# Kernel tuning notes

Hardware: AMD Instinct MI355X
Metric: run time of the kernel (lower is better)

Reference implementation:

```python
import jax, jax.numpy as jnp
from jax import lax
import numpy as np

D_IN = 512    # inputdim
HID = 128     # hiddendim
D_INNER = 2 * HID   # 256
D_PROJ = 2 * D_INNER  # 512
N_STATE = 16
R_DT = 8      # ceil(128/16)
B, H, W = 8, 32, 32


def _layernorm(y, g, b):
    mu = y.mean(-1, keepdims=True)
    var = ((y - mu) ** 2).mean(-1, keepdims=True)
    return (y - mu) / jnp.sqrt(var + 1e-5) * g + b


def _ssm(x, xw, dtw, dtb, Al, Dv, g, be):
    # x: [B, D, L] -> y: [B, L, D]  (Mamba selective scan, delta_softplus=True)
    Bb, D, L = x.shape
    n = Al.shape[1]
    xd = jnp.einsum('bdl,kd->blk', x, xw)             # [B,L,R+2N]
    dts = xd[..., :R_DT]
    Bs = xd[..., R_DT:R_DT + n]                        # [B,L,N]
    Cs = xd[..., R_DT + n:]                            # [B,L,N]
    delta = jax.nn.softplus(jnp.einsum('blr,dr->bld', dts, dtw) + dtb)  # [B,L,D]
    A = -jnp.exp(Al)                                   # [D,N]
    xt = x.transpose(0, 2, 1)                          # [B,L,D]
    dA = jnp.exp(delta[..., None] * A)                 # [B,L,D,N]
    dBx = delta[..., None] * Bs[:, :, None, :] * xt[..., None]  # [B,L,D,N]

    def step(h, inp):
        da, dbx, c = inp
        h = h * da + dbx
        return h, jnp.einsum('bdn,bn->bd', h, c)

    h0 = jnp.zeros((Bb, D, n), x.dtype)
    _, ys = lax.scan(step, h0, (dA.transpose(1, 0, 2, 3),
                                dBx.transpose(1, 0, 2, 3),
                                Cs.transpose(1, 0, 2)))
    y = ys.transpose(1, 0, 2) + xt * Dv                # [B,L,D]
    return _layernorm(y, g, be)


def _up2(y, h, w):
    Bb, L, C = y.shape
    img = y.transpose(0, 2, 1).reshape(Bb, C, h, w)
    img = jnp.repeat(jnp.repeat(img, 2, axis=2), 2, axis=3)
    return img.reshape(Bb, C, 4 * L).transpose(0, 2, 1)


def _conv1x1(x, w, b):
    return jnp.einsum('bchw,oc->bohw', x, w) + b[None, :, None, None]


def _conv2s2(x, w, b):
    out = lax.conv_general_dilated(x, w, (2, 2), 'VALID',
                                   dimension_numbers=('NCHW', 'OIHW', 'NCHW'))
    return out + b[None, :, None, None]


def _forward(input_f, in_w, in_b, c1_w, c1_b, c2_w, c2_b, c3_w, c3_b, out_w, out_b,
             xw1, dtw1, dtb1, Al1, Dv1, g1, be1,
             xw2, dtw2, dtb2, Al2, Dv2, g2, be2,
             xw3, dtw3, dtb3, Al3, Dv3, g3, be3):
    xz = _conv1x1(input_f, in_w, in_b)
    x, z = jnp.split(xz, 2, axis=1)
    f1 = _conv1x1(x, c1_w, c1_b)                      # [B,256,H,W]
    f2 = _conv2s2(f1, c2_w, c2_b)                     # [B,256,H/2,W/2]
    f3 = _conv2s2(f2, c3_w, c3_b)                     # [B,256,H/4,W/4]

    Bb, C, h3, w3 = f3.shape
    fx3 = f3.reshape(Bb, C, h3 * w3)
    y3 = _ssm(fx3, xw3, dtw3, dtb3, Al3, Dv3, g3, be3) + \
         jnp.flip(_ssm(jnp.flip(fx3, -1), xw3, dtw3, dtb3, Al3, Dv3, g3, be3), 1)
    y2_ = _up2(y3, h3, w3)

    _, _, h2, w2 = f2.shape
    fx2 = f2.reshape(Bb, C, h2 * w2)
    y2 = _ssm(fx2, xw2, dtw2, dtb2, Al2, Dv2, g2, be2) + \
         jnp.flip(_ssm(jnp.flip(fx2, -1), xw2, dtw2, dtb2, Al2, Dv2, g2, be2), 1) + y2_
    y1_ = _up2(y2, h2, w2)

    _, _, h1, w1 = f1.shape
    fx1 = f1.reshape(Bb, C, h1 * w1)
    # NOTE: source uses fssm1 forward and fssm2 on the flipped sequence
    y1 = _ssm(fx1, xw1, dtw1, dtb1, Al1, Dv1, g1, be1) + \
         jnp.flip(_ssm(jnp.flip(fx1, -1), xw2, dtw2, dtb2, Al2, Dv2, g2, be2), 1) + y1_

    out1 = y1.transpose(0, 2, 1).reshape(Bb, C, h1, w1)
    out = out1 * jax.nn.silu(z)
    return _conv1x1(out, out_w, out_b)


def setup_inputs() -> dict:
    key = jax.random.key(0)
    ks = iter(jax.random.split(key, 64))
    def nrm(shape, s=0.05):
        return (jax.random.normal(next(ks), shape, dtype=jnp.float32) * s)
    inp = {
        'input_f': jax.random.normal(next(ks), (B, D_IN, H, W), dtype=jnp.float32),
        'in_w': nrm((D_PROJ, D_IN)), 'in_b': nrm((D_PROJ,)),
        'c1_w': nrm((D_INNER, D_INNER)), 'c1_b': nrm((D_INNER,)),
        'c2_w': nrm((D_INNER, D_INNER, 2, 2)), 'c2_b': nrm((D_INNER,)),
        'c3_w': nrm((D_INNER, D_INNER, 2, 2)), 'c3_b': nrm((D_INNER,)),
        'out_w': nrm((D_IN, D_INNER)), 'out_b': nrm((D_IN,)),
    }
    Al = jnp.log(jnp.tile(jnp.arange(1, N_STATE + 1, dtype=jnp.float32), (D_INNER, 1)))
    for i in (1, 2, 3):
        inp[f'xw{i}'] = nrm((R_DT + 2 * N_STATE, D_INNER))
        inp[f'dtw{i}'] = nrm((D_INNER, R_DT), s=R_DT ** -0.5)
        inp[f'dtb{i}'] = nrm((D_INNER,)) - 4.0   # inv-softplus of small dt
        inp[f'Al{i}'] = Al
        inp[f'Dv{i}'] = jnp.ones((D_INNER,), jnp.float32)
        inp[f'g{i}'] = jnp.ones((D_INNER,), jnp.float32)
        inp[f'be{i}'] = jnp.zeros((D_INNER,), jnp.float32)
    return inp


def reference(input_f, in_w, in_b, c1_w, c1_b, c2_w, c2_b, c3_w, c3_b, out_w, out_b,
              xw1, dtw1, dtb1, Al1, Dv1, g1, be1,
              xw2, dtw2, dtb2, Al2, Dv2, g2, be2,
              xw3, dtw3, dtb3, Al3, Dv3, g3, be3):
    return _forward(input_f, in_w, in_b, c1_w, c1_b, c2_w, c2_b, c3_w, c3_b, out_w, out_b,
                    xw1, dtw1, dtb1, Al1, Dv1, g1, be1,
                    xw2, dtw2, dtb2, Al2, Dv2, g2, be2,
                    xw3, dtw3, dtb3, Al3, Dv3, g3, be3)
```

## Files before the change

kernel.cpp:

```cpp
#include <hip/hip_runtime.h>
#include <cstddef>

#define DEV static __device__ __forceinline__

typedef __attribute__((ext_vector_type(8))) short short8;
typedef __attribute__((ext_vector_type(4))) float floatx4;

DEV float siluf(float v) { return v / (1.f + expf(-v)); }

DEV unsigned short f2bf(float f) {
  unsigned int u = __float_as_uint(f);
  u += 0x7fff + ((u >> 16) & 1);
  return (unsigned short)(u >> 16);
}

template <int AMT>
DEV float ror_add(float v) {
  int s = __builtin_amdgcn_update_dpp(0, __float_as_int(v), 0x120 | AMT, 0xF, 0xF, false);
  return v + __int_as_float(s);
}

__global__ __launch_bounds__(256) void cvt_w_k(
    const float* __restrict__ in_w, const float* __restrict__ c1_w,
    const float* __restrict__ c2_w, const float* __restrict__ c3_w,
    const float* __restrict__ out_w, const float* __restrict__ xw1,
    const float* __restrict__ xw2, const float* __restrict__ xw3,
    unsigned short* __restrict__ wsW)
{
  int gid = blockIdx.x * 256 + threadIdx.x;
  float v;
  if      (gid < 262144)  v = in_w[gid];
  else if (gid < 327680)  v = c1_w[gid - 262144];
  else if (gid < 589824)  {
    int off = gid - 327680;
    int o = off >> 10, kk = off & 1023, ij = kk >> 8, c = kk & 255;
    v = c2_w[o * 1024 + c * 4 + ij];
  }
  else if (gid < 851968)  {
    int off = gid - 589824;
    int o = off >> 10, kk = off & 1023, ij = kk >> 8, c = kk & 255;
    v = c3_w[o * 1024 + c * 4 + ij];
  }
  else if (gid < 983040)  v = out_w[gid - 851968];
  else if (gid < 993280)  v = xw1[gid - 983040];
  else if (gid < 1003520) v = xw2[gid - 993280];
  else                    v = xw3[gid - 1003520];
  wsW[gid] = f2bf(v);
}

__global__ __launch_bounds__(256) void tcvt_k(const float* __restrict__ in,
                                              unsigned short* __restrict__ outp,
                                              int C, int L)
{
  __shared__ float tile[32][33];
  int b = blockIdx.y;
  int nLt = L >> 5;
  int pt = blockIdx.x % nLt, ct = blockIdx.x / nLt;
  int p0 = pt * 32, c0 = ct * 32;
  int r = threadIdx.x >> 5, cc = threadIdx.x & 31;
#pragma unroll
  for (int i = 0; i < 4; i++) {
    int row = r + 8 * i;
    tile[row][cc] = in[((size_t)b * C + c0 + row) * L + p0 + cc];
  }
  __syncthreads();
#pragma unroll
  for (int i = 0; i < 4; i++) {
    int row = r + 8 * i;
    outp[((size_t)b * L + p0 + row) * C + c0 + cc] = f2bf(tile[cc][row]);
  }
}

__global__ __launch_bounds__(256) void im2col2_k(const unsigned short* __restrict__ f1t,
                                                 unsigned short* __restrict__ outp)
{
  int idx = blockIdx.x * 256 + threadIdx.x;
  int cs = idx & 31, ij = (idx >> 5) & 3, n = (idx >> 7) & 255, b = idx >> 15;
  int i = ij >> 1, j = ij & 1;
  int y = n >> 4, x = n & 15;
  int pix = (2 * y + i) * 32 + 2 * x + j;
  uint4 v = *(const uint4*)&f1t[((size_t)b * 1024 + pix) * 256 + cs * 8];
  *(uint4*)&outp[((size_t)b * 256 + n) * 1024 + ij * 256 + cs * 8] = v;
}

__global__ __launch_bounds__(256) void im2col3_k(const unsigned short* __restrict__ f2t,
                                                 unsigned short* __restrict__ outp)
{
  int idx = blockIdx.x * 256 + threadIdx.x;
  int cs = idx & 31, ij = (idx >> 5) & 3, n = (idx >> 7) & 63, b = idx >> 13;
  int i = ij >> 1, j = ij & 1;
  int y = n >> 3, x = n & 7;
  int pix = (2 * y + i) * 16 + 2 * x + j;
  uint4 v = *(const uint4*)&f2t[((size_t)b * 256 + pix) * 256 + cs * 8];
  *(uint4*)&outp[((size_t)b * 64 + n) * 1024 + ij * 256 + cs * 8] = v;
}

template <int EPI>
__global__ __launch_bounds__(256) void mgemm_k(
    const unsigned short* __restrict__ A, long long sA,
    const unsigned short* __restrict__ B, long long sB,
    const float* __restrict__ bias, float* __restrict__ Y0,
    unsigned short* __restrict__ Yt, float* __restrict__ Ys,
    int M, int N, int K, int Mt, int Nt)
{
  __shared__ __align__(16) unsigned short Ab[128 * 40];
  __shared__ __align__(16) unsigned short Bb[128 * 40];
  int bid = blockIdx.x;
  int tiles = Mt * Nt;
  int bb = bid / tiles;
  int rr = bid - bb * tiles;
  int m0 = (rr / Nt) * 128;
  int n0 = (rr % Nt) * 128;
  const unsigned short* Ap = A + (size_t)bb * sA;
  const unsigned short* Bp = B + (size_t)bb * sB;

  int t = threadIdx.x;
  int lane = t & 63;
  int wm = ((t >> 7) & 1) * 64;
  int wn = ((t >> 6) & 1) * 64;
  int l15 = lane & 15, quad = lane >> 4;

  int srow = t >> 1;
  int shalf = (t & 1) * 16;
  int arow = m0 + srow; if (arow > M - 1) arow = M - 1;
  int brow = n0 + srow; if (brow > N - 1) brow = N - 1;
  const unsigned short* ap = Ap + (size_t)arow * K + shalf;
  const unsigned short* bp = Bp + (size_t)brow * K + shalf;
  unsigned short* as = &Ab[srow * 40 + shalf];
  unsigned short* bs = &Bb[srow * 40 + shalf];

  floatx4 acc[4][4] = {};

  for (int k0 = 0; k0 < K; k0 += 32) {
    uint4 a0 = *(const uint4*)(ap + k0);
    uint4 a1 = *(const uint4*)(ap + k0 + 8);
    uint4 b0 = *(const uint4*)(bp + k0);
    uint4 b1 = *(const uint4*)(bp + k0 + 8);
    __syncthreads();
    *(uint4*)as = a0; *(uint4*)(as + 8) = a1;
    *(uint4*)bs = b0; *(uint4*)(bs + 8) = b1;
    __syncthreads();
    short8 af[4], bf[4];
#pragma unroll
    for (int i = 0; i < 4; i++)
      af[i] = *(const short8*)&Ab[(wm + i * 16 + l15) * 40 + quad * 8];
#pragma unroll
    for (int j = 0; j < 4; j++)
      bf[j] = *(const short8*)&Bb[(wn + j * 16 + l15) * 40 + quad * 8];
#pragma unroll
    for (int i = 0; i < 4; i++)
#pragma unroll
      for (int j = 0; j < 4; j++)
        acc[i][j] = __builtin_amdgcn_mfma_f32_16x16x32_bf16(af[i], bf[j],
                                                            acc[i][j], 0, 0, 0);
  }

  if (EPI == 1) {
    float bn[4]; int nn[4];
#pragma unroll
    for (int j = 0; j < 4; j++) { nn[j] = n0 + wn + j * 16 + l15; bn[j] = bias[nn[j]]; }
#pragma unroll
    for (int i = 0; i < 4; i++) {
      int pixb = m0 + wm + i * 16 + quad * 4;
#pragma unroll
      for (int j = 0; j < 4; j++) {
        int n = nn[j];
        if (n < 256) {
#pragma unroll
          for (int r = 0; r < 4; r++)
            Yt[((size_t)bb * 1024 + pixb + r) * 256 + n] = f2bf(acc[i][j][r] + bn[j]);
        } else {
#pragma unroll
          for (int r = 0; r < 4; r++)
            Ys[((size_t)bb * 1024 + pixb + r) * 256 + (n - 256)] =
                siluf(acc[i][j][r] + bn[j]);
        }
      }
    }
  } else {
#pragma unroll
    for (int i = 0; i < 4; i++) {
      int m = m0 + wm + i * 16 + quad * 4;
#pragma unroll
      for (int j = 0; j < 4; j++) {
        int n = n0 + wn + j * 16 + l15;
        if (m < M && n < N) {
          float vr[4];
#pragma unroll
          for (int r = 0; r < 4; r++)
            vr[r] = acc[i][j][r] + (bias ? bias[m + r] : 0.f);
          float* yp = &Y0[((size_t)bb * M + m) * N + n];
#pragma unroll
          for (int r = 0; r < 4; r++) yp[(size_t)r * N] = vr[r];
          if (EPI == 2) {
            ushort4 o;
            o.x = f2bf(vr[0]); o.y = f2bf(vr[1]); o.z = f2bf(vr[2]); o.w = f2bf(vr[3]);
            *(ushort4*)&Yt[((size_t)bb * N + n) * M + m] = o;
          }
        }
      }
    }
  }
}

__global__ __launch_bounds__(256) void post_all_k(
    const float* __restrict__ xd12, const float* __restrict__ xd2,
    const float* __restrict__ xd3,
    const float* __restrict__ dtw1, const float* __restrict__ dtb1,
    const float* __restrict__ dtw2, const float* __restrict__ dtb2,
    const float* __restrict__ dtw3, const float* __restrict__ dtb3,
    float* __restrict__ d1f, float* __restrict__ bc1f,
    float* __restrict__ d1b, float* __restrict__ bc1b,
    float* __restrict__ d2g, float* __restrict__ bc2,
    float* __restrict__ d3g, float* __restrict__ bc3)
{
  int bid = blockIdx.x;
  const float* xd; int bstride, L; const float *dtw, *dtb; float *dg, *bg;
  int lt, b;
  if (bid < 512) {
    int r = bid; lt = r & 63; b = r >> 6;
    xd = xd12; bstride = 80 * 1024; L = 1024; dtw = dtw1; dtb = dtb1; dg = d1f; bg = bc1f;
  } else if (bid < 1024) {
    int r = bid - 512; lt = r & 63; b = r >> 6;
    xd = xd12 + 40 * 1024; bstride = 80 * 1024; L = 1024; dtw = dtw2; dtb = dtb2; dg = d1b; bg = bc1b;
  } else if (bid < 1152) {
    int r = bid - 1024; lt = r & 15; b = r >> 4;
    xd = xd2; bstride = 40 * 256; L = 256; dtw = dtw2; dtb = dtb2; dg = d2g; bg = bc2;
  } else {
    int r = bid - 1152; lt = r & 3; b = r >> 2;
    xd = xd3; bstride = 40 * 64; L = 64; dtw = dtw3; dtb = dtb3; dg = d3g; bg = bc3;
  }
  int l0 = lt * 16;
  __shared__ float dl[8][16];
  int t = threadIdx.x;
  const float* xb = xd + (size_t)b * bstride + l0;
  if (t < 128) {
    int r = t >> 4, l = t & 15;
    dl[r][l] = xb[(size_t)r * L + l];
  } else {
    int tt = t - 128;
    int c = tt >> 2, seg = tt & 3;
    float4 v = *(const float4*)&xb[(size_t)(8 + c) * L + seg * 4];
    *(float4*)&bg[((size_t)b * 32 + c) * L + l0 + seg * 4] = v;
  }
  __syncthreads();
  int d = t;
  float dtwv[8];
#pragma unroll
  for (int r = 0; r < 8; r++) dtwv[r] = dtw[d * 8 + r];
  float dtbv = dtb[d];
  float spv[16];
#pragma unroll
  for (int l = 0; l < 16; l++) {
    float s = dtbv;
#pragma unroll
    for (int r = 0; r < 8; r++) s += dl[r][l] * dtwv[r];
    spv[l] = fmaxf(s, 0.f) + log1pf(expf(-fabsf(s)));
  }
  float* dout = dg + ((size_t)b * 256 + d) * L + l0;
#pragma unroll
  for (int i = 0; i < 4; i++)
    *(float4*)&dout[4 * i] = make_float4(spv[4 * i], spv[4 * i + 1],
                                         spv[4 * i + 2], spv[4 * i + 3]);
}

#define SCAN_STEPA(DVV, DXV, BVV) {                \
    float e_ = __expf((DVV) * A);                  \
    h = h * e_ + (BVV) * (DXV);                    \
    P *= e_; }

__global__ __launch_bounds__(256) void scanA_k(
    const float* __restrict__ f1, const float* __restrict__ f2,
    const float* __restrict__ d1f, const float* __restrict__ bc1f,
    const float* __restrict__ d1b, const float* __restrict__ bc1b,
    const float* __restrict__ d2,  const float* __restrict__ bc2,
    const float* __restrict__ Al1, const float* __restrict__ Al2,
    float* __restrict__ cP, float* __restrict__ cQ)
{
  __shared__ __align__(16) float lds[48][68];
  int bid = blockIdx.x;
  int sid, tseg, L; const float *xin, *dlp, *bcp, *Alp;
  if (bid < 4096) {
    sid = bid >> 4; tseg = bid & 15; L = 1024; xin = f1;
    if (((sid >> 4) & 1) == 0) { dlp = d1f; bcp = bc1f; Alp = Al1; }
    else                       { dlp = d1b; bcp = bc1b; Alp = Al2; }
  } else {
    int idx = bid - 4096; sid = idx >> 2; tseg = idx & 3; L = 256;
    xin = f2; dlp = d2; bcp = bc2; Alp = Al2;
  }
  int b = sid >> 5, dir = (sid >> 4) & 1, g = sid & 15;
  int t = threadIdx.x, n = t & 15, dloc = t >> 4, d = g * 16 + dloc;
  int mbase = dir ? (L - 64 * (tseg + 1)) : 64 * tseg;

  int r0 = t >> 4, cs = t & 15;
  {
    const float* p0 = dlp + ((size_t)b * 256 + g * 16 + r0) * L + mbase;
    const float* p1 = xin + ((size_t)b * 256 + g * 16 + r0) * L + mbase;
    const float* p2 = bcp + ((size_t)b * 32 + r0) * L + mbase;
    float4 v0 = *(const float4*)(p0 + cs * 4);
    float4 v1 = *(const float4*)(p1 + cs * 4);
    float4 v2 = *(const float4*)(p2 + cs * 4);
    float4 dx = make_float4(v0.x * v1.x, v0.y * v1.y, v0.z * v1.z, v0.w * v1.w);
    *(float4*)&lds[r0][cs * 4]      = v0;
    *(float4*)&lds[16 + r0][cs * 4] = dx;
    *(float4*)&lds[32 + r0][cs * 4] = v2;
  }
  __syncthreads();

  float A = -expf(Alp[d * 16 + n]);
  float h = 0.f, P = 1.f;
  if (dir == 0) {
#pragma unroll
    for (int g4 = 0; g4 < 16; g4++) {
      int cb = 4 * g4;
      float4 dv4 = *(const float4*)&lds[dloc][cb];
      float4 dx4 = *(const float4*)&lds[16 + dloc][cb];
      float4 bv4 = *(const float4*)&lds[32 + n][cb];
      SCAN_STEPA(dv4.x, dx4.x, bv4.x);
      SCAN_STEPA(dv4.y, dx4.y, bv4.y);
      SCAN_STEPA(dv4.z, dx4.z, bv4.z);
      SCAN_STEPA(dv4.w, dx4.w, bv4.w);
    }
  } else {
#pragma unroll
    for (int g4 = 0; g4 < 16; g4++) {
      int cb = 60 - 4 * g4;
      float4 dv4 = *(const float4*)&lds[dloc][cb];
      float4 dx4 = *(const float4*)&lds[16 + dloc][cb];
      float4 bv4 = *(const float4*)&lds[32 + n][cb];
      SCAN_STEPA(dv4.w, dx4.w, bv4.w);
      SCAN_STEPA(dv4.z, dx4.z, bv4.z);
      SCAN_STEPA(dv4.y, dx4.y, bv4.y);
      SCAN_STEPA(dv4.x, dx4.x, bv4.x);
    }
  }
  cP[(size_t)bid * 256 + t] = P;
  cQ[(size_t)bid * 256 + t] = h;
}

__global__ __launch_bounds__(256) void scanB_k(float* __restrict__ cP,
                                               const float* __restrict__ cQ)
{
  int bidx = blockIdx.x, t = threadIdx.x;
  int S, base;
  if (bidx < 256) { S = 16; base = bidx * 16; }
  else            { S = 4;  base = 4096 + (bidx - 256) * 4; }
  float h = 0.f;
  for (int s = 0; s < S; s++) {
    size_t off = (size_t)(base + s) * 256 + t;
    float p = cP[off], q = cQ[off];
    cP[off] = h;
    h = p * h + q;
  }
}

#define SCAN_STEPY(DVV, DXV, BVV, CVV, COL) {      \
    float e_ = __expf((DVV) * A);                  \
    h = h * e_ + (BVV) * (DXV);                    \
    float pp_ = h * (CVV);                         \
    pp_ = ror_add<1>(pp_);                         \
    pp_ = ror_add<2>(pp_);                         \
    pp_ = ror_add<4>(pp_);                         \
    pp_ = ror_add<8>(pp_);                         \
    ysel = (((COL) & 15) == n) ? pp_ : ysel; }

__global__ __launch_bounds__(256) void scanC_k(
    const float* __restrict__ f1, const float* __restrict__ f2, const float* __restrict__ f3,
    const float* __restrict__ d1f, const float* __restrict__ bc1f,
    const float* __restrict__ d1b, const float* __restrict__ bc1b,
    const float* __restrict__ d2,  const float* __restrict__ bc2,
    const float* __restrict__ d3,  const float* __restrict__ bc3,
    float* __restrict__ y1f, float* __restrict__ y1b,
    float* __restrict__ y2f, float* __restrict__ y2b,
    float* __restrict__ y3f, float* __restrict__ y3b,
    const float* __restrict__ Al1, const float* __restrict__ Dv1,
    const float* __restrict__ Al2, const float* __restrict__ Dv2,
    const float* __restrict__ Al3, const float* __restrict__ Dv3,
    const float* __restrict__ cP)
{
  __shared__ __align__(16) float lds[80][68];
  int bid = blockIdx.x;
  int sid, tseg, L, slot; const float *xin, *dlp, *bcp, *Alp, *Dvp; float* yo;
  if (bid < 4096) {
    sid = bid >> 4; tseg = bid & 15; slot = bid; L = 1024; xin = f1;
    if (((sid >> 4) & 1) == 0) { dlp = d1f; bcp = bc1f; Alp = Al1; Dvp = Dv1; yo = y1f; }
    else                       { dlp = d1b; bcp = bc1b; Alp = Al2; Dvp = Dv2; yo = y1b; }
  } else if (bid < 5120) {
    int idx = bid - 4096; sid = idx >> 2; tseg = idx & 3; slot = bid; L = 256;
    xin = f2; dlp = d2; bcp = bc2; Alp = Al2; Dvp = Dv2;
    yo = ((sid >> 4) & 1) ? y2b : y2f;
  } else {
    sid = bid - 5120; tseg = 0; slot = -1; L = 64;
    xin = f3; dlp = d3; bcp = bc3; Alp = Al3; Dvp = Dv3;
    yo = ((sid >> 4) & 1) ? y3b : y3f;
  }
  int b = sid >> 5, dir = (sid >> 4) & 1, g = sid & 15;
  int t = threadIdx.x, n = t & 15, dloc = t >> 4, d = g * 16 + dloc;
  int mbase = dir ? (L - 64 * (tseg + 1)) : 64 * tseg;

  int r0 = t >> 4, cs = t & 15;
  {
    const float* p0 = dlp + ((size_t)b * 256 + g * 16 + r0) * L + mbase;
    const float* p1 = xin + ((size_t)b * 256 + g * 16 + r0) * L + mbase;
    const float* p2 = bcp + ((size_t)b * 32 + r0) * L + mbase;
    const float* p3 = bcp + ((size_t)b * 32 + 16 + r0) * L + mbase;
    float4 v0 = *(const float4*)(p0 + cs * 4);
    float4 v1 = *(const float4*)(p1 + cs * 4);
    float4 v2 = *(const float4*)(p2 + cs * 4);
    float4 v3 = *(const float4*)(p3 + cs * 4);
    float4 dx = make_float4(v0.x * v1.x, v0.y * v1.y, v0.z * v1.z, v0.w * v1.w);
    *(float4*)&lds[r0][cs * 4]      = v0;
    *(float4*)&lds[16 + r0][cs * 4] = dx;
    *(float4*)&lds[32 + r0][cs * 4] = v1;
    *(float4*)&lds[48 + r0][cs * 4] = v2;
    *(float4*)&lds[64 + r0][cs * 4] = v3;
  }
  float A   = -expf(Alp[d * 16 + n]);
  float Dvv = Dvp[d];
  float h = (slot >= 0) ? cP[(size_t)slot * 256 + t] : 0.f;
  __syncthreads();

  float* ybase = yo + ((size_t)b * L + mbase) * 256 + d;
#pragma unroll
  for (int jj0 = 0; jj0 < 64; jj0 += 16) {
    float ysel = 0.f;
    if (dir == 0) {
#pragma unroll
      for (int g4 = 0; g4 < 4; g4++) {
        int cb = jj0 + 4 * g4;
        float4 dv4 = *(const float4*)&lds[dloc][cb];
        float4 dx4 = *(const float4*)&lds[16 + dloc][cb];
        float4 bv4 = *(const float4*)&lds[48 + n][cb];
        float4 cv4 = *(const float4*)&lds[64 + n][cb];
        SCAN_STEPY(dv4.x, dx4.x, bv4.x, cv4.x, cb + 0);
        SCAN_STEPY(dv4.y, dx4.y, bv4.y, cv4.y, cb + 1);
        SCAN_STEPY(dv4.z, dx4.z, bv4.z, cv4.z, cb + 2);
        SCAN_STEPY(dv4.w, dx4.w, bv4.w, cv4.w, cb + 3);
      }
    } else {
#pragma unroll
      for (int g4 = 0; g4 < 4; g4++) {
        int cb = 60 - jj0 - 4 * g4;
        float4 dv4 = *(const float4*)&lds[dloc][cb];
        float4 dx4 = *(const float4*)&lds[16 + dloc][cb];
        float4 bv4 = *(const float4*)&lds[48 + n][cb];
        float4 cv4 = *(const float4*)&lds[64 + n][cb];
        SCAN_STEPY(dv4.w, dx4.w, bv4.w, cv4.w, cb + 3);
        SCAN_STEPY(dv4.z, dx4.z, bv4.z, cv4.z, cb + 2);
        SCAN_STEPY(dv4.y, dx4.y, bv4.y, cv4.y, cb + 1);
        SCAN_STEPY(dv4.x, dx4.x, bv4.x, cv4.x, cb + 0);
      }
    }
    int colbase = dir ? 48 - jj0 : jj0;
    float xsel = lds[32 + dloc][colbase + n];
    ybase[(size_t)(colbase + n) * 256] = ysel + xsel * Dvv;
  }
}

template <int OUTBF>
__global__ __launch_bounds__(256) void ln_combine(
    const float* __restrict__ yf, const float* __restrict__ yb,
    const float* __restrict__ gf, const float* __restrict__ bef,
    const float* __restrict__ gb, const float* __restrict__ beb,
    const float* __restrict__ up, int Wc,
    const float* __restrict__ szT, void* __restrict__ outv,
    int L, int Wf)
{
  int bid = blockIdx.x;
  int b = bid / L;
  int l = bid - b * L;
  int d = threadIdx.x;
  size_t base = ((size_t)b * L + l) * 256 + d;
  float vf = yf[base], vb = yb[base];
  float4 s = make_float4(vf, vf * vf, vb, vb * vb);
#pragma unroll
  for (int m = 1; m < 64; m <<= 1) {
    s.x += __shfl_xor(s.x, m);
    s.y += __shfl_xor(s.y, m);
    s.z += __shfl_xor(s.z, m);
    s.w += __shfl_xor(s.w, m);
  }
  __shared__ float red[4][4];
  int w = threadIdx.x >> 6;
  if ((threadIdx.x & 63) == 0) {
    red[w][0] = s.x; red[w][1] = s.y; red[w][2] = s.z; red[w][3] = s.w;
  }
  __syncthreads();
  float s0 = red[0][0] + red[1][0] + red[2][0] + red[3][0];
  float s1 = red[0][1] + red[1][1] + red[2][1] + red[3][1];
  float s2 = red[0][2] + red[1][2] + red[2][2] + red[3][2];
  float s3 = red[0][3] + red[1][3] + red[2][3] + red[3][3];
  const float inv = 1.f / 256.f;
  float muf = s0 * inv, varf = s1 * inv - muf * muf;
  float mub = s2 * inv, varb = s3 * inv - mub * mub;
  float rf = rsqrtf(varf + 1e-5f);
  float rb = rsqrtf(varb + 1e-5f);
  float v = (vf - muf) * rf * gf[d] + bef[d] + (vb - mub) * rb * gb[d] + beb[d];
  if (up) {
    int y = l / Wf, x = l - y * Wf;
    int lc = (y >> 1) * Wc + (x >> 1);
    v += up[((size_t)b * (L >> 2) + lc) * 256 + d];
  }
  if (szT) v *= szT[base];
  if (OUTBF) ((unsigned short*)outv)[base] = f2bf(v);
  else       ((float*)outv)[base] = v;
}

extern "C" void kernel_launch(void* const* d_in, const int* in_sizes, int n_in,
                              void* d_out, int out_size, void* d_ws, size_t ws_size,
                              hipStream_t stream) {
  (void)in_sizes; (void)n_in; (void)out_size; (void)ws_size;
  const float* input_f = (const float*)d_in[0];
  const float* in_w  = (const float*)d_in[1];
  const float* in_b  = (const float*)d_in[2];
  const float* c1_w  = (const float*)d_in[3];
  const float* c1_b  = (const float*)d_in[4];
  const float* c2_w  = (const float*)d_in[5];
  const float* c2_b  = (const float*)d_in[6];
  const float* c3_w  = (const float*)d_in[7];
  const float* c3_b  = (const float*)d_in[8];
  const float* out_w = (const float*)d_in[9];
  const float* out_b = (const float*)d_in[10];
  const float* xw1  = (const float*)d_in[11];
  const float* dtw1 = (const float*)d_in[12];
  const float* dtb1 = (const float*)d_in[13];
  const float* Al1  = (const float*)d_in[14];
  const float* Dv1  = (const float*)d_in[15];
  const float* g1   = (const float*)d_in[16];
  const float* be1  = (const float*)d_in[17];
  const float* xw2  = (const float*)d_in[18];
  const float* dtw2 = (const float*)d_in[19];
  const float* dtb2 = (const float*)d_in[20];
  const float* Al2  = (const float*)d_in[21];
  const float* Dv2  = (const float*)d_in[22];
  const float* g2   = (const float*)d_in[23];
  const float* be2  = (const float*)d_in[24];
  const float* xw3  = (const float*)d_in[25];
  const float* dtw3 = (const float*)d_in[26];
  const float* dtb3 = (const float*)d_in[27];
  const float* Al3  = (const float*)d_in[28];
  const float* Dv3  = (const float*)d_in[29];
  const float* g3   = (const float*)d_in[30];
  const float* be3  = (const float*)d_in[31];

  float* ws = (float*)d_ws;
  constexpr size_t M1 = 2097152;
  float* d1f = ws;
  unsigned short* xt = (unsigned short*)(ws + M1);
  float* y1f = ws + M1;
  float* szT = ws + 2 * M1;
  float* f1  = ws + 3 * M1;
  unsigned short* G = (unsigned short*)(ws + 3 * M1);
  float* d1b = ws + 4 * M1;
  unsigned short* inT = (unsigned short*)(ws + 5 * M1);
  unsigned short* ic2 = inT;
  unsigned short* f1t = inT + 2097152;
  unsigned short* ic3 = f1t;
  float* y1b = ws + 5 * M1;
  size_t o = 6 * M1;
  float* f2   = ws + o; o += 524288;
  float* f3   = ws + o; o += 131072;
  float* bc1f = ws + o; o += 262144;
  float* bc1b = ws + o; o += 262144;
  float* d2   = ws + o; o += 524288;
  float* bc2  = ws + o; o += 65536;
  float* d3   = ws + o; o += 131072;
  float* bc3  = ws + o; o += 16384;
  float* y2f  = ws + o; o += 524288;
  float* y2b  = ws + o; o += 524288;
  float* y3f  = ws + o; o += 131072;
  float* y3b  = ws + o; o += 131072;
  float* y3c  = ws + o; o += 131072;
  float* y2c  = ws + o; o += 524288;
  float* cP   = ws + o; o += 1310720;
  float* cQ   = ws + o; o += 1310720;
  unsigned short* wsW = (unsigned short*)(ws + o); o += 506880;
  float* xd12 = cP;
  float* xd2  = cP + 655360;
  float* xd3  = cP + 737280;
  unsigned short* f2t = (unsigned short*)cQ;
  unsigned short* f3t = (unsigned short*)(cQ + 262144);
  unsigned short* w_in   = wsW;
  unsigned short* w_c1   = wsW + 262144;
  unsigned short* w_c2   = wsW + 327680;
  unsigned short* w_c3   = wsW + 589824;
  unsigned short* w_out  = wsW + 851968;
  unsigned short* w_xw12 = wsW + 983040;
  unsigned short* w_xw2  = wsW + 993280;
  unsigned short* w_xw3  = wsW + 1003520;

  dim3 blk(256);

  cvt_w_k<<<dim3(3960), blk, 0, stream>>>(in_w, c1_w, c2_w, c3_w, out_w,
                                          xw1, xw2, xw3, wsW);
  tcvt_k<<<dim3(512, 8), blk, 0, stream>>>(input_f, inT, 512, 1024);
  mgemm_k<1><<<dim3(256), blk, 0, stream>>>(inT, 1024 * 512, w_in, 0, in_b,
                                            nullptr, xt, szT, 1024, 512, 512, 8, 4);
  mgemm_k<2><<<dim3(128), blk, 0, stream>>>(w_c1, 0, xt, 1024 * 256, c1_b,
                                            f1, f1t, nullptr, 256, 1024, 256, 2, 8);
  mgemm_k<0><<<dim3(64), blk, 0, stream>>>(w_xw12, 0, f1t, 1024 * 256, nullptr,
                                           xd12, nullptr, nullptr, 80, 1024, 256, 1, 8);
  im2col2_k<<<dim3(1024), blk, 0, stream>>>(f1t, ic2);
  mgemm_k<2><<<dim3(32), blk, 0, stream>>>(w_c2, 0, ic2, 256 * 1024, c2_b,
                                           f2, f2t, nullptr, 256, 256, 1024, 2, 2);
  im2col3_k<<<dim3(256), blk, 0, stream>>>(f2t, ic3);
  mgemm_k<2><<<dim3(16), blk, 0, stream>>>(w_c3, 0, ic3, 64 * 1024, c3_b,
                                           f3, f3t, nullptr, 256, 64, 1024, 2, 1);
  mgemm_k<0><<<dim3(16), blk, 0, stream>>>(w_xw2, 0, f2t, 256 * 256, nullptr,
                                           xd2, nullptr, nullptr, 40, 256, 256, 1, 2);
  mgemm_k<0><<<dim3(8), blk, 0, stream>>>(w_xw3, 0, f3t, 64 * 256, nullptr,
                                          xd3, nullptr, nullptr, 40, 64, 256, 1, 1);
  post_all_k<<<dim3(1184), blk, 0, stream>>>(xd12, xd2, xd3,
                                             dtw1, dtb1, dtw2, dtb2, dtw3, dtb3,
                                             d1f, bc1f, d1b, bc1b, d2, bc2, d3, bc3);
  scanA_k<<<dim3(5120), blk, 0, stream>>>(f1, f2, d1f, bc1f, d1b, bc1b,
                                          d2, bc2, Al1, Al2, cP, cQ);
  scanB_k<<<dim3(512), blk, 0, stream>>>(cP, cQ);
  scanC_k<<<dim3(5376), blk, 0, stream>>>(f1, f2, f3,
                                          d1f, bc1f, d1b, bc1b, d2, bc2, d3, bc3,
                                          y1f, y1b, y2f, y2b, y3f, y3b,
                                          Al1, Dv1, Al2, Dv2, Al3, Dv3, cP);
  ln_combine<0><<<dim3(512), blk, 0, stream>>>(y3f, y3b, g3, be3, g3, be3,
                                               nullptr, 0, nullptr, y3c, 64, 8);
  ln_combine<0><<<dim3(2048), blk, 0, stream>>>(y2f, y2b, g2, be2, g2, be2,
                                                y3c, 8, nullptr, y2c, 256, 16);
  ln_combine<1><<<dim3(8192), blk, 0, stream>>>(y1f, y1b, g1, be1, g2, be2,
                                                y2c, 16, szT, G, 1024, 32);
  mgemm_k<0><<<dim3(256), blk, 0, stream>>>(w_out, 0, G, 1024 * 256, out_b,
                                            (float*)d_out, nullptr, nullptr,
                                            512, 1024, 256, 4, 8);
}
```

Measured before the change: 387.2 us.

## Merge small launches, store activations in bf16, fold carry combine into scan

Merges the weight-conversion and input-transpose kernels into one launch. Runs the im2col copies inside the same launches as the small xd GEMMs. Stores the f1/f2/f3 conv outputs and the SiLU gate as bf16 instead of fp32, which halves their memory traffic. Drops the scanB kernel: each scanC block now combines the preceding segment carries itself and recovers x as dx/delta instead of keeping a separate x tile in LDS. This cuts launch count and bandwidth, but adds redundant serial carry work per block and some extra precision loss from bf16 storage and the division.

```diff
diff --git a/kernel.cpp b/kernel.cpp
--- a/kernel.cpp
+++ b/kernel.cpp
@@ -13,6 +13,12 @@
   u += 0x7fff + ((u >> 16) & 1);
   return (unsigned short)(u >> 16);
 }
+DEV float bf2f(unsigned short u) {
+  return __uint_as_float(((unsigned int)u) << 16);
+}
+DEV float4 bf2f4(ushort4 v) {
+  return make_float4(bf2f(v.x), bf2f(v.y), bf2f(v.z), bf2f(v.w));
+}
 
 template <int AMT>
 DEV float ror_add(float v) {
@@ -20,92 +26,66 @@
   return v + __int_as_float(s);
 }
 
-__global__ __launch_bounds__(256) void cvt_w_k(
+__global__ __launch_bounds__(256) void prep_k(
     const float* __restrict__ in_w, const float* __restrict__ c1_w,
     const float* __restrict__ c2_w, const float* __restrict__ c3_w,
     const float* __restrict__ out_w, const float* __restrict__ xw1,
     const float* __restrict__ xw2, const float* __restrict__ xw3,
-    unsigned short* __restrict__ wsW)
-{
-  int gid = blockIdx.x * 256 + threadIdx.x;
-  float v;
-  if      (gid < 262144)  v = in_w[gid];
-  else if (gid < 327680)  v = c1_w[gid - 262144];
-  else if (gid < 589824)  {
-    int off = gid - 327680;
-    int o = off >> 10, kk = off & 1023, ij = kk >> 8, c = kk & 255;
-    v = c2_w[o * 1024 + c * 4 + ij];
-  }
-  else if (gid < 851968)  {
-    int off = gid - 589824;
-    int o = off >> 10, kk = off & 1023, ij = kk >> 8, c = kk & 255;
-    v = c3_w[o * 1024 + c * 4 + ij];
-  }
-  else if (gid < 983040)  v = out_w[gid - 851968];
-  else if (gid < 993280)  v = xw1[gid - 983040];
-  else if (gid < 1003520) v = xw2[gid - 993280];
-  else                    v = xw3[gid - 1003520];
-  wsW[gid] = f2bf(v);
-}
-
-__global__ __launch_bounds__(256) void tcvt_k(const float* __restrict__ in,
-                                              unsigned short* __restrict__ outp,
-                                              int C, int L)
+    unsigned short* __restrict__ wsW,
+    const float* __restrict__ input_f, unsigned short* __restrict__ inT)
 {
   __shared__ float tile[32][33];
-  int b = blockIdx.y;
-  int nLt = L >> 5;
-  int pt = blockIdx.x % nLt, ct = blockIdx.x / nLt;
-  int p0 = pt * 32, c0 = ct * 32;
-  int r = threadIdx.x >> 5, cc = threadIdx.x & 31;
-#pragma unroll
-  for (int i = 0; i < 4; i++) {
-    int row = r + 8 * i;
-    tile[row][cc] = in[((size_t)b * C + c0 + row) * L + p0 + cc];
-  }
-  __syncthreads();
-#pragma unroll
-  for (int i = 0; i < 4; i++) {
-    int row = r + 8 * i;
-    outp[((size_t)b * L + p0 + row) * C + c0 + cc] = f2bf(tile[cc][row]);
-  }
-}
-
-__global__ __launch_bounds__(256) void im2col2_k(const unsigned short* __restrict__ f1t,
-                                                 unsigned short* __restrict__ outp)
-{
-  int idx = blockIdx.x * 256 + threadIdx.x;
-  int cs = idx & 31, ij = (idx >> 5) & 3, n = (idx >> 7) & 255, b = idx >> 15;
-  int i = ij >> 1, j = ij & 1;
-  int y = n >> 4, x = n & 15;
-  int pix = (2 * y + i) * 32 + 2 * x + j;
-  uint4 v = *(const uint4*)&f1t[((size_t)b * 1024 + pix) * 256 + cs * 8];
-  *(uint4*)&outp[((size_t)b * 256 + n) * 1024 + ij * 256 + cs * 8] = v;
-}
-
-__global__ __launch_bounds__(256) void im2col3_k(const unsigned short* __restrict__ f2t,
-                                                 unsigned short* __restrict__ outp)
-{
-  int idx = blockIdx.x * 256 + threadIdx.x;
-  int cs = idx & 31, ij = (idx >> 5) & 3, n = (idx >> 7) & 63, b = idx >> 13;
-  int i = ij >> 1, j = ij & 1;
-  int y = n >> 3, x = n & 7;
-  int pix = (2 * y + i) * 16 + 2 * x + j;
-  uint4 v = *(const uint4*)&f2t[((size_t)b * 256 + pix) * 256 + cs * 8];
-  *(uint4*)&outp[((size_t)b * 64 + n) * 1024 + ij * 256 + cs * 8] = v;
+  int bid = blockIdx.x;
+  int t = threadIdx.x;
+  if (bid < 3960) {
+    int gid = bid * 256 + t;
+    float v;
+    if      (gid < 262144)  v = in_w[gid];
+    else if (gid < 327680)  v = c1_w[gid - 262144];
+    else if (gid < 589824)  {
+      int off = gid - 327680;
+      int o = off >> 10, kk = off & 1023, ij = kk >> 8, c = kk & 255;
+      v = c2_w[o * 1024 + c * 4 + ij];
+    }
+    else if (gid < 851968)  {
+      int off = gid - 589824;
+      int o = off >> 10, kk = off & 1023, ij = kk >> 8, c = kk & 255;
+      v = c3_w[o * 1024 + c * 4 + ij];
+    }
+    else if (gid < 983040)  v = out_w[gid - 851968];
+    else if (gid < 993280)  v = xw1[gid - 983040];
+    else if (gid < 1003520) v = xw2[gid - 993280];
+    else                    v = xw3[gid - 1003520];
+    wsW[gid] = f2bf(v);
+  } else {
+    int idx = bid - 3960;
+    int b = idx >> 9, blk = idx & 511;
+    int pt = blk & 31, ct = blk >> 5;
+    int p0 = pt * 32, c0 = ct * 32;
+    int r = t >> 5, cc = t & 31;
+#pragma unroll
+    for (int i = 0; i < 4; i++) {
+      int row = r + 8 * i;
+      tile[row][cc] = input_f[((size_t)b * 512 + c0 + row) * 1024 + p0 + cc];
+    }
+    __syncthreads();
+#pragma unroll
+    for (int i = 0; i < 4; i++) {
+      int row = r + 8 * i;
+      inT[((size_t)b * 1024 + p0 + row) * 512 + c0 + cc] = f2bf(tile[cc][row]);
+    }
+  }
 }
 
 template <int EPI>
-__global__ __launch_bounds__(256) void mgemm_k(
-    const unsigned short* __restrict__ A, long long sA,
-    const unsigned short* __restrict__ B, long long sB,
-    const float* __restrict__ bias, float* __restrict__ Y0,
-    unsigned short* __restrict__ Yt, float* __restrict__ Ys,
-    int M, int N, int K, int Mt, int Nt)
+DEV void mgemm_body(const unsigned short* __restrict__ A, long long sA,
+                    const unsigned short* __restrict__ B, long long sB,
+                    const float* __restrict__ bias,
+                    void* __restrict__ O1, void* __restrict__ O2,
+                    int M, int N, int K, int Mt, int Nt, int bid)
 {
   __shared__ __align__(16) unsigned short Ab[128 * 40];
   __shared__ __align__(16) unsigned short Bb[128 * 40];
-  int bid = blockIdx.x;
   int tiles = Mt * Nt;
   int bb = bid / tiles;
   int rr = bid - bb * tiles;
@@ -156,6 +136,8 @@
   }
 
   if (EPI == 1) {
+    unsigned short* Yt = (unsigned short*)O1;
+    unsigned short* Ys = (unsigned short*)O2;
     float bn[4]; int nn[4];
 #pragma unroll
     for (int j = 0; j < 4; j++) { nn[j] = n0 + wn + j * 16 + l15; bn[j] = bias[nn[j]]; }
@@ -173,7 +155,7 @@
 #pragma unroll
           for (int r = 0; r < 4; r++)
             Ys[((size_t)bb * 1024 + pixb + r) * 256 + (n - 256)] =
-                siluf(acc[i][j][r] + bn[j]);
+                f2bf(siluf(acc[i][j][r] + bn[j]));
         }
       }
     }
@@ -189,10 +171,17 @@
 #pragma unroll
           for (int r = 0; r < 4; r++)
             vr[r] = acc[i][j][r] + (bias ? bias[m + r] : 0.f);
-          float* yp = &Y0[((size_t)bb * M + m) * N + n];
-#pragma unroll
-          for (int r = 0; r < 4; r++) yp[(size_t)r * N] = vr[r];
-          if (EPI == 2) {
+          if (EPI == 0) {
+            float* Y0 = (float*)O1;
+            float* yp = &Y0[((size_t)bb * M + m) * N + n];
+#pragma unroll
+            for (int r = 0; r < 4; r++) yp[(size_t)r * N] = vr[r];
+          } else {
+            unsigned short* Y0b = (unsigned short*)O1;
+            unsigned short* Yt  = (unsigned short*)O2;
+#pragma unroll
+            for (int r = 0; r < 4; r++)
+              Y0b[((size_t)bb * M + m + r) * N + n] = f2bf(vr[r]);
             ushort4 o;
             o.x = f2bf(vr[0]); o.y = f2bf(vr[1]); o.z = f2bf(vr[2]); o.w = f2bf(vr[3]);
             *(ushort4*)&Yt[((size_t)bb * N + n) * M + m] = o;
@@ -200,6 +189,54 @@
         }
       }
     }
+  }
+}
+
+template <int EPI>
+__global__ __launch_bounds__(256) void mgemm_k(
+    const unsigned short* __restrict__ A, long long sA,
+    const unsigned short* __restrict__ B, long long sB,
+    const float* __restrict__ bias, void* __restrict__ O1, void* __restrict__ O2,
+    int M, int N, int K, int Mt, int Nt)
+{
+  mgemm_body<EPI>(A, sA, B, sB, bias, O1, O2, M, N, K, Mt, Nt, blockIdx.x);
+}
+
+__global__ __launch_bounds__(256) void fat1_k(
+    const unsigned short* __restrict__ w_xw12, const unsigned short* __restrict__ f1t,
+    float* __restrict__ xd12, unsigned short* __restrict__ ic2)
+{
+  int bid = blockIdx.x;
+  if (bid < 64) {
+    mgemm_body<0>(w_xw12, 0, f1t, 1024 * 256, nullptr, xd12, nullptr,
+                  80, 1024, 256, 1, 8, bid);
+  } else {
+    int idx = (bid - 64) * 256 + threadIdx.x;
+    int cs = idx & 31, ij = (idx >> 5) & 3, n = (idx >> 7) & 255, b = idx >> 15;
+    int i = ij >> 1, j = ij & 1;
+    int y = n >> 4, x = n & 15;
+    int pix = (2 * y + i) * 32 + 2 * x + j;
+    uint4 v = *(const uint4*)&f1t[((size_t)b * 1024 + pix) * 256 + cs * 8];
+    *(uint4*)&ic2[((size_t)b * 256 + n) * 1024 + ij * 256 + cs * 8] = v;
+  }
+}
+
+__global__ __launch_bounds__(256) void fat2_k(
+    const unsigned short* __restrict__ w_xw2, const unsigned short* __restrict__ f2t,
+    float* __restrict__ xd2, unsigned short* __restrict__ ic3)
+{
+  int bid = blockIdx.x;
+  if (bid < 16) {
+    mgemm_body<0>(w_xw2, 0, f2t, 256 * 256, nullptr, xd2, nullptr,
+                  40, 256, 256, 1, 2, bid);
+  } else {
+    int idx = (bid - 16) * 256 + threadIdx.x;
+    int cs = idx & 31, ij = (idx >> 5) & 3, n = (idx >> 7) & 63, b = idx >> 13;
+    int i = ij >> 1, j = ij & 1;
+    int y = n >> 3, x = n & 7;
+    int pix = (2 * y + i) * 16 + 2 * x + j;
+    uint4 v = *(const uint4*)&f2t[((size_t)b * 256 + pix) * 256 + cs * 8];
+    *(uint4*)&ic3[((size_t)b * 64 + n) * 1024 + ij * 256 + cs * 8] = v;
   }
 }
 
@@ -270,7 +307,7 @@
     P *= e_; }
 
 __global__ __launch_bounds__(256) void scanA_k(
-    const float* __restrict__ f1, const float* __restrict__ f2,
+    const unsigned short* __restrict__ f1b, const unsigned short* __restrict__ f2b,
     const float* __restrict__ d1f, const float* __restrict__ bc1f,
     const float* __restrict__ d1b, const float* __restrict__ bc1b,
     const float* __restrict__ d2,  const float* __restrict__ bc2,
@@ -279,14 +316,14 @@
 {
   __shared__ __align__(16) float lds[48][68];
   int bid = blockIdx.x;
-  int sid, tseg, L; const float *xin, *dlp, *bcp, *Alp;
+  int sid, tseg, L; const unsigned short* xin; const float *dlp, *bcp, *Alp;
   if (bid < 4096) {
-    sid = bid >> 4; tseg = bid & 15; L = 1024; xin = f1;
+    sid = bid >> 4; tseg = bid & 15; L = 1024; xin = f1b;
     if (((sid >> 4) & 1) == 0) { dlp = d1f; bcp = bc1f; Alp = Al1; }
     else                       { dlp = d1b; bcp = bc1b; Alp = Al2; }
   } else {
     int idx = bid - 4096; sid = idx >> 2; tseg = idx & 3; L = 256;
-    xin = f2; dlp = d2; bcp = bc2; Alp = Al2;
+    xin = f2b; dlp = d2; bcp = bc2; Alp = Al2;
   }
   int b = sid >> 5, dir = (sid >> 4) & 1, g = sid & 15;
   int t = threadIdx.x, n = t & 15, dloc = t >> 4, d = g * 16 + dloc;
@@ -295,12 +332,12 @@
   int r0 = t >> 4, cs = t & 15;
   {
     const float* p0 = dlp + ((size_t)b * 256 + g * 16 + r0) * L + mbase;
-    const float* p1 = xin + ((size_t)b * 256 + g * 16 + r0) * L + mbase;
+    const unsigned short* p1 = xin + ((size_t)b * 256 + g * 16 + r0) * L + mbase;
     const float* p2 = bcp + ((size_t)b * 32 + r0) * L + mbase;
     float4 v0 = *(const float4*)(p0 + cs * 4);
-    float4 v1 = *(const float4*)(p1 + cs * 4);
+    float4 xf = bf2f4(*(const ushort4*)(p1 + cs * 4));
     float4 v2 = *(const float4*)(p2 + cs * 4);
-    float4 dx = make_float4(v0.x * v1.x, v0.y * v1.y, v0.z * v1.z, v0.w * v1.w);
+    float4 dx = make_float4(v0.x * xf.x, v0.y * xf.y, v0.z * xf.z, v0.w * xf.w);
     *(float4*)&lds[r0][cs * 4]      = v0;
     *(float4*)&lds[16 + r0][cs * 4] = dx;
     *(float4*)&lds[32 + r0][cs * 4] = v2;
@@ -338,22 +375,6 @@
   cQ[(size_t)bid * 256 + t] = h;
 }
 
-__global__ __launch_bounds__(256) void scanB_k(float* __restrict__ cP,
-                                               const float* __restrict__ cQ)
-{
-  int bidx = blockIdx.x, t = threadIdx.x;
-  int S, base;
-  if (bidx < 256) { S = 16; base = bidx * 16; }
-  else            { S = 4;  base = 4096 + (bidx - 256) * 4; }
-  float h = 0.f;
-  for (int s = 0; s < S; s++) {
-    size_t off = (size_t)(base + s) * 256 + t;
-    float p = cP[off], q = cQ[off];
-    cP[off] = h;
-    h = p * h + q;
-  }
-}
-
 #define SCAN_STEPY(DVV, DXV, BVV, CVV, COL) {      \
     float e_ = __expf((DVV) * A);                  \
     h = h * e_ + (BVV) * (DXV);                    \
@@ -365,7 +386,8 @@
     ysel = (((COL) & 15) == n) ? pp_ : ysel; }
 
 __global__ __launch_bounds__(256) void scanC_k(
-    const float* __restrict__ f1, const float* __restrict__ f2, const float* __restrict__ f3,
+    const unsigned short* __restrict__ f1b, const unsigned short* __restrict__ f2b,
+    const unsigned short* __restrict__ f3b,
     const float* __restrict__ d1f, const float* __restrict__ bc1f,
     const float* __restrict__ d1b, const float* __restrict__ bc1b,
     const float* __restrict__ d2,  const float* __restrict__ bc2,
@@ -376,22 +398,23 @@
     const float* __restrict__ Al1, const float* __restrict__ Dv1,
     const float* __restrict__ Al2, const float* __restrict__ Dv2,
     const float* __restrict__ Al3, const float* __restrict__ Dv3,
-    const float* __restrict__ cP)
-{
-  __shared__ __align__(16) float lds[80][68];
+    const float* __restrict__ cP, const float* __restrict__ cQ)
+{
+  __shared__ __align__(16) float lds[64][68];
   int bid = blockIdx.x;
-  int sid, tseg, L, slot; const float *xin, *dlp, *bcp, *Alp, *Dvp; float* yo;
+  int sid, tseg, L, sbase; const unsigned short* xin;
+  const float *dlp, *bcp, *Alp, *Dvp; float* yo;
   if (bid < 4096) {
-    sid = bid >> 4; tseg = bid & 15; slot = bid; L = 1024; xin = f1;
+    sid = bid >> 4; tseg = bid & 15; sbase = sid * 16; L = 1024; xin = f1b;
     if (((sid >> 4) & 1) == 0) { dlp = d1f; bcp = bc1f; Alp = Al1; Dvp = Dv1; yo = y1f; }
     else                       { dlp = d1b; bcp = bc1b; Alp = Al2; Dvp = Dv2; yo = y1b; }
   } else if (bid < 5120) {
-    int idx = bid - 4096; sid = idx >> 2; tseg = idx & 3; slot = bid; L = 256;
-    xin = f2; dlp = d2; bcp = bc2; Alp = Al2; Dvp = Dv2;
+    int idx = bid - 4096; sid = idx >> 2; tseg = idx & 3; sbase = 4096 + sid * 4;
+    L = 256; xin = f2b; dlp = d2; bcp = bc2; Alp = Al2; Dvp = Dv2;
     yo = ((sid >> 4) & 1) ? y2b : y2f;
   } else {
-    sid = bid - 5120; tseg = 0; slot = -1; L = 64;
-    xin = f3; dlp = d3; bcp = bc3; Alp = Al3; Dvp = Dv3;
+    sid = bid - 5120; tseg = 0; sbase = -1; L = 64;
+    xin = f3b; dlp = d3; bcp = bc3; Alp = Al3; Dvp = Dv3;
     yo = ((sid >> 4) & 1) ? y3b : y3f;
   }
   int b = sid >> 5, dir = (sid >> 4) & 1, g = sid & 15;
@@ -401,23 +424,28 @@
   int r0 = t >> 4, cs = t & 15;
   {
     const float* p0 = dlp + ((size_t)b * 256 + g * 16 + r0) * L + mbase;
-    const float* p1 = xin + ((size_t)b * 256 + g * 16 + r0) * L + mbase;
+    const unsigned short* p1 = xin + ((size_t)b * 256 + g * 16 + r0) * L + mbase;
     const float* p2 = bcp + ((size_t)b * 32 + r0) * L + mbase;
     const float* p3 = bcp + ((size_t)b * 32 + 16 + r0) * L + mbase;
     float4 v0 = *(const float4*)(p0 + cs * 4);
-    float4 v1 = *(const float4*)(p1 + cs * 4);
+    float4 xf = bf2f4(*(const ushort4*)(p1 + cs * 4));
     float4 v2 = *(const float4*)(p2 + cs * 4);
     float4 v3 = *(const float4*)(p3 + cs * 4);
-    float4 dx = make_float4(v0.x * v1.x, v0.y * v1.y, v0.z * v1.z, v0.w * v1.w);
+    float4 dx = make_float4(v0.x * xf.x, v0.y * xf.y, v0.z * xf.z, v0.w * xf.w);
     *(float4*)&lds[r0][cs * 4]      = v0;
     *(float4*)&lds[16 + r0][cs * 4] = dx;
-    *(float4*)&lds[32 + r0][cs * 4] = v1;
-    *(float4*)&lds[48 + r0][cs * 4] = v2;
-    *(float4*)&lds[64 + r0][cs * 4] = v3;
+    *(float4*)&lds[32 + r0][cs * 4] = v2;
+    *(float4*)&lds[48 + r0][cs * 4] = v3;
   }
   float A   = -expf(Alp[d * 16 + n]);
   float Dvv = Dvp[d];
-  float h = (slot >= 0) ? cP[(size_t)slot * 256 + t] : 0.f;
+  float h = 0.f;
+  if (sbase >= 0) {
+    for (int s = 0; s < tseg; ++s) {
+      size_t off = (size_t)(sbase + s) * 256 + t;
+      h = cP[off] * h + cQ[off];
+    }
+  }
   __syncthreads();
 
   float* ybase = yo + ((size_t)b * L + mbase) * 256 + d;
@@ -430,8 +458,8 @@
         int cb = jj0 + 4 * g4;
         float4 dv4 = *(const float4*)&lds[dloc][cb];
         float4 dx4 = *(const float4*)&lds[16 + dloc][cb];
-        float4 bv4 = *(const float4*)&lds[48 + n][cb];
-        float4 cv4 = *(const float4*)&lds[64 + n][cb];
+        float4 bv4 = *(const float4*)&lds[32 + n][cb];
+        float4 cv4 = *(const float4*)&lds[48 + n][cb];
         SCAN_STEPY(dv4.x, dx4.x, bv4.x, cv4.x, cb + 0);
         SCAN_STEPY(dv4.y, dx4.y, bv4.y, cv4.y, cb + 1);
         SCAN_STEPY(dv4.z, dx4.z, bv4.z, cv4.z, cb + 2);
@@ -443,8 +471,8 @@
         int cb = 60 - jj0 - 4 * g4;
         float4 dv4 = *(const float4*)&lds[dloc][cb];
         float4 dx4 = *(const float4*)&lds[16 + dloc][cb];
-        float4 bv4 = *(const float4*)&lds[48 + n][cb];
-        float4 cv4 = *(const float4*)&lds[64 + n][cb];
+        float4 bv4 = *(const float4*)&lds[32 + n][cb];
+        float4 cv4 = *(const float4*)&lds[48 + n][cb];
         SCAN_STEPY(dv4.w, dx4.w, bv4.w, cv4.w, cb + 3);
         SCAN_STEPY(dv4.z, dx4.z, bv4.z, cv4.z, cb + 2);
         SCAN_STEPY(dv4.y, dx4.y, bv4.y, cv4.y, cb + 1);
@@ -452,7 +480,9 @@
       }
     }
     int colbase = dir ? 48 - jj0 : jj0;
-    float xsel = lds[32 + dloc][colbase + n];
+    float dsel  = lds[dloc][colbase + n];
+    float dxsel = lds[16 + dloc][colbase + n];
+    float xsel  = dxsel / fmaxf(dsel, 1e-30f);
     ybase[(size_t)(colbase + n) * 256] = ysel + xsel * Dvv;
   }
 }
@@ -463,7 +493,7 @@
     const float* __restrict__ gf, const float* __restrict__ bef,
     const float* __restrict__ gb, const float* __restrict__ beb,
     const float* __restrict__ up, int Wc,
-    const float* __restrict__ szT, void* __restrict__ outv,
+    const unsigned short* __restrict__ szb, void* __restrict__ outv,
     int L, int Wf)
 {
   int bid = blockIdx.x;
@@ -501,7 +531,7 @@
     int lc = (y >> 1) * Wc + (x >> 1);
     v += up[((size_t)b * (L >> 2) + lc) * 256 + d];
   }
-  if (szT) v *= szT[base];
+  if (szb) v *= bf2f(szb[base]);
   if (OUTBF) ((unsigned short*)outv)[base] = f2bf(v);
   else       ((float*)outv)[base] = v;
 }
@@ -548,9 +578,9 @@
   float* d1f = ws;
   unsigned short* xt = (unsigned short*)(ws + M1);
   float* y1f = ws + M1;
-  float* szT = ws + 2 * M1;
-  float* f1  = ws + 3 * M1;
-  unsigned short* G = (unsigned short*)(ws + 3 * M1);
+  unsigned short* szb = (unsigned short*)(ws + 2 * M1);
+  unsigned short* f1b = (unsigned short*)(ws + 3 * M1);
+  unsigned short* G = (unsigned short*)(ws + 3 * M1) + 2097152;
   float* d1b = ws + 4 * M1;
   unsigned short* inT = (unsigned short*)(ws + 5 * M1);
   unsigned short* ic2 = inT;
@@ -558,8 +588,8 @@
   unsigned short* ic3 = f1t;
   float* y1b = ws + 5 * M1;
   size_t o = 6 * M1;
-  float* f2   = ws + o; o += 524288;
-  float* f3   = ws + o; o += 131072;
+  unsigned short* f2b = (unsigned short*)(ws + o); o += 524288;
+  unsigned short* f3b = (unsigned short*)(ws + o); o += 131072;
   float* bc1f = ws + o; o += 262144;
   float* bc1b = ws + o; o += 262144;
   float* d2   = ws + o; o += 524288;
@@ -591,42 +621,36 @@
 
   dim3 blk(256);
 
-  cvt_w_k<<<dim3(3960), blk, 0, stream>>>(in_w, c1_w, c2_w, c3_w, out_w,
-                                          xw1, xw2, xw3, wsW);
-  tcvt_k<<<dim3(512, 8), blk, 0, stream>>>(input_f, inT, 512, 1024);
+  prep_k<<<dim3(8056), blk, 0, stream>>>(in_w, c1_w, c2_w, c3_w, out_w,
+                                         xw1, xw2, xw3, wsW, input_f, inT);
   mgemm_k<1><<<dim3(256), blk, 0, stream>>>(inT, 1024 * 512, w_in, 0, in_b,
-                                            nullptr, xt, szT, 1024, 512, 512, 8, 4);
-  mgemm_k<2><<<dim3(128), blk, 0, stream>>>(w_c1, 0, xt, 1024 * 256, c1_b,
-                                            f1, f1t, nullptr, 256, 1024, 256, 2, 8);
-  mgemm_k<0><<<dim3(64), blk, 0, stream>>>(w_xw12, 0, f1t, 1024 * 256, nullptr,
-                                           xd12, nullptr, nullptr, 80, 1024, 256, 1, 8);
-  im2col2_k<<<dim3(1024), blk, 0, stream>>>(f1t, ic2);
-  mgemm_k<2><<<dim3(32), blk, 0, stream>>>(w_c2, 0, ic2, 256 * 1024, c2_b,
-                                           f2, f2t, nullptr, 256, 256, 1024, 2, 2);
-  im2col3_k<<<dim3(256), blk, 0, stream>>>(f2t, ic3);
-  mgemm_k<2><<<dim3(16), blk, 0, stream>>>(w_c3, 0, ic3, 64 * 1024, c3_b,
-                                           f3, f3t, nullptr, 256, 64, 1024, 2, 1);
-  mgemm_k<0><<<dim3(16), blk, 0, stream>>>(w_xw2, 0, f2t, 256 * 256, nullptr,
-                                           xd2, nullptr, nullptr, 40, 256, 256, 1, 2);
+                                            xt, szb, 1024, 512, 512, 8, 4);
+  mgemm_k<3><<<dim3(128), blk, 0, stream>>>(w_c1, 0, xt, 1024 * 256, c1_b,
+                                            f1b, f1t, 256, 1024, 256, 2, 8);
+  fat1_k<<<dim3(1088), blk, 0, stream>>>(w_xw12, f1t, xd12, ic2);
+  mgemm_k<3><<<dim3(32), blk, 0, stream>>>(w_c2, 0, ic2, 256 * 1024, c2_b,
+                                           f2b, f2t, 256, 256, 1024, 2, 2);
+  fat2_k<<<dim3(272), blk, 0, stream>>>(w_xw2, f2t, xd2, ic3);
+  mgemm_k<3><<<dim3(16), blk, 0, stream>>>(w_c3, 0, ic3, 64 * 1024, c3_b,
+                                           f3b, f3t, 256, 64, 1024, 2, 1);
   mgemm_k<0><<<dim3(8), blk, 0, stream>>>(w_xw3, 0, f3t, 64 * 256, nullptr,
-                                          xd3, nullptr, nullptr, 40, 64, 256, 1, 1);
+                                          xd3, nullptr, 40, 64, 256, 1, 1);
   post_all_k<<<dim3(1184), blk, 0, stream>>>(xd12, xd2, xd3,
                                              dtw1, dtb1, dtw2, dtb2, dtw3, dtb3,
                                              d1f, bc1f, d1b, bc1b, d2, bc2, d3, bc3);
-  scanA_k<<<dim3(5120), blk, 0, stream>>>(f1, f2, d1f, bc1f, d1b, bc1b,
+  scanA_k<<<dim3(5120), blk, 0, stream>>>(f1b, f2b, d1f, bc1f, d1b, bc1b,
                                           d2, bc2, Al1, Al2, cP, cQ);
-  scanB_k<<<dim3(512), blk, 0, stream>>>(cP, cQ);
-  scanC_k<<<dim3(5376), blk, 0, stream>>>(f1, f2, f3,
+  scanC_k<<<dim3(5376), blk, 0, stream>>>(f1b, f2b, f3b,
                                           d1f, bc1f, d1b, bc1b, d2, bc2, d3, bc3,
                                           y1f, y1b, y2f, y2b, y3f, y3b,
-                                          Al1, Dv1, Al2, Dv2, Al3, Dv3, cP);
+                                          Al1, Dv1, Al2, Dv2, Al3, Dv3, cP, cQ);
   ln_combine<0><<<dim3(512), blk, 0, stream>>>(y3f, y3b, g3, be3, g3, be3,
                                                nullptr, 0, nullptr, y3c, 64, 8);
   ln_combine<0><<<dim3(2048), blk, 0, stream>>>(y2f, y2b, g2, be2, g2, be2,
                                                 y3c, 8, nullptr, y2c, 256, 16);
   ln_combine<1><<<dim3(8192), blk, 0, stream>>>(y1f, y1b, g1, be1, g2, be2,
-                                                y2c, 16, szT, G, 1024, 32);
+                                                y2c, 16, szb, G, 1024, 32);
   mgemm_k<0><<<dim3(256), blk, 0, stream>>>(w_out, 0, G, 1024 * 256, out_b,
-                                            (float*)d_out, nullptr, nullptr,
+                                            (float*)d_out, nullptr,
                                             512, 1024, 256, 4, 8);
 }
```

New measurement: 377.3 us. -2.6%, faster.
